# Performance work log

Hardware: AMD Instinct MI355X
Metric: run time of the kernel (lower is better)

Reference implementation:

```python
import jax, jax.numpy as jnp
import numpy as np

N, E, G = 100000, 600000, 64  # nodes, edges, graphs
F_IN, W, EPS = 32, 128, 1e-5


def setup_inputs() -> dict:
    key = jax.random.key(0)
    ks = jax.random.split(key, 16)
    p = lambda k, shape: jax.random.normal(k, shape, dtype=jnp.float32) * 0.1
    z = lambda n: jnp.zeros((n,), jnp.float32)
    o = lambda n: jnp.ones((n,), jnp.float32)
    return {
        "x": jax.random.normal(ks[0], (N, F_IN), dtype=jnp.float32),
        "edge_index": jax.random.randint(ks[1], (2, E), 0, N, dtype=jnp.int32),
        "batch": jnp.sort(jax.random.randint(ks[2], (N,), 0, G, dtype=jnp.int32)),
        # GCNConv layers
        "W1": p(ks[3], (F_IN, W)), "b1": z(W),
        "W2": p(ks[4], (W, W)), "b2": z(W),
        # mlp_first: Linear -> BN -> ReLU -> Linear
        "W3": p(ks[5], (W, W)), "b3": z(W), "g1": o(W), "be1": z(W),
        "W4": p(ks[6], (W, W)), "b4": z(W),
        # mlp: Linear -> BN -> ReLU -> Linear
        "W5": p(ks[7], (W, W // 2)), "b5": z(W // 2), "g2": o(W // 2), "be2": z(W // 2),
        "W6": p(ks[8], (W // 2, 1)), "b6": z(1),
    }


def gcn_conv(x, src, dst, Wt, b):
    # PyG GCNConv with add_self_loops=True: D^-1/2 (A+I) D^-1/2 (x W) + b
    h = x @ Wt  # [N, width]
    deg = jax.ops.segment_sum(jnp.ones(src.shape[0], x.dtype), dst, num_segments=N) + 1.0
    dinv = jax.lax.rsqrt(deg)
    norm = dinv[src] * dinv[dst]  # per-edge normalization
    agg = jax.ops.segment_sum(h[src] * norm[:, None], dst, num_segments=N)
    # self-loop term: norm for (i,i) is 1/deg[i]
    return agg + h * (dinv * dinv)[:, None] + b


def batch_norm(x, g, b):
    # training-mode BatchNorm1d (batch stats, biased var)
    mu = x.mean(axis=0)
    var = jnp.mean((x - mu) ** 2, axis=0)
    return (x - mu) * jax.lax.rsqrt(var + EPS) * g + b


def reference(x, edge_index, batch, W1, b1, W2, b2, W3, b3, g1, be1, W4, b4, W5, b5, g2, be2, W6, b6):
    src, dst = edge_index[0], edge_index[1]
    x = jax.nn.relu(gcn_conv(x, src, dst, W1, b1))
    x = jax.nn.relu(gcn_conv(x, src, dst, W2, b2))
    # mlp_first + ReLU
    x = jax.nn.relu(batch_norm(x @ W3 + b3, g1, be1)) @ W4 + b4
    x = jax.nn.relu(x)
    # global max pool over nodes per graph
    x = jax.ops.segment_max(x, batch, num_segments=G)  # [G, width]
    # final mlp
    x = jax.nn.relu(batch_norm(x @ W5 + b5, g2, be2)) @ W6 + b6
    return x[:, 0]
```

## Files before the change

### kernel.cpp

```cpp
#include <hip/hip_runtime.h>

#define N_NODES 100000
#define N_EDGES 600000
#define N_GRAPHS 64
#define EPS 1e-5f
#define SCAN_BLOCKS 391

typedef unsigned short u16;
typedef unsigned int u32;
typedef __attribute__((ext_vector_type(8))) short bf16x8;
typedef __attribute__((ext_vector_type(4))) float f32x4;

__device__ __forceinline__ float bf2f(u16 u) { return __uint_as_float(((u32)u) << 16); }
__device__ __forceinline__ u16 f2bf(float f) {
    u32 u = __float_as_uint(f);
    u += 0x7FFFu + ((u >> 16) & 1u);
    return (u16)(u >> 16);
}
__device__ __forceinline__ float2 bfx2(u32 v) {
    float2 r;
    r.x = __uint_as_float(v << 16);
    r.y = __uint_as_float(v & 0xFFFF0000u);
    return r;
}

#define WS_COUNTS   ((size_t)0)
#define WS_CURSOR   ((size_t)400384)
#define WS_POOLED   ((size_t)800768)
#define WS_BNSUM    ((size_t)833536)
#define WS_BNSUMSQ  ((size_t)834048)
#define WS_FLAG     ((size_t)834560)
#define ZERO_BYTES  ((size_t)835072)
#define WS_OFFSETS  ((size_t)835072)
#define WS_DINV     ((size_t)1235456)
#define WS_DINV2    ((size_t)1635840)
#define WS_SRCS     ((size_t)2036224)
#define WS_ZF       ((size_t)4436736)
#define WS_CANONW   ((size_t)4453120)
#define WS_BUFA     ((size_t)4578560)
#define WS_BUFB     ((size_t)30178560)

#define CW_W1 0
#define CW_B1 4096
#define CW_W2 4224
#define CW_B2 20608
#define CW_W3 20736
#define CW_B3 37120
#define CW_G1 37248
#define CW_BE1 37376
#define CW_W4 37504
#define CW_B4 53888
#define CW_W5 54016
#define CW_B5 62208
#define CW_G2 62272
#define CW_BE2 62336
#define CW_W6 62400
#define CW_B6 62464

__global__ void detect_kernel(const u32* __restrict__ xraw, int* __restrict__ flag) {
    __shared__ int cnt;
    if (threadIdx.x == 0) cnt = 0;
    __syncthreads();
    int c = 0;
    for (int i = threadIdx.x; i < 2048; i += 256) {
        u32 w = xraw[i];
        float a = fabsf(__uint_as_float((w & 0xFFFFu) << 16));
        if (a == 0.f || (a > 1e-8f && a < 1e4f)) c++;
    }
    atomicAdd(&cnt, c);
    __syncthreads();
    if (threadIdx.x == 0) *flag = (cnt > 1024) ? 1 : 0;
}

__global__ void convx_kernel(const void* __restrict__ xsrc, u16* __restrict__ dst,
                             const int* __restrict__ flag, const float* __restrict__ dinv) {
    int i = blockIdx.x * 256 + threadIdx.x;
    if (i < N_NODES * 32) {
        int r = i >> 5, c = i & 31;
        float v = (*flag) ? bf2f(((const u16*)xsrc)[i]) : ((const float*)xsrc)[i];
        dst[(size_t)(c >> 3) * (N_NODES * 8) + (size_t)r * 8 + (c & 7)] = f2bf(v * dinv[r]);
    }
}

struct SmallArgs {
    const void* src[16];
    int n[16];
    int off[16];
    int cols[16];
};
__global__ void convs_kernel(SmallArgs a, u16* __restrict__ dst, const int* __restrict__ flag) {
    int i = blockIdx.x * 256 + threadIdx.x;
    int isbf = *flag;
#pragma unroll
    for (int j = 0; j < 16; j++)
        if (i < a.n[j]) {
            u16 v = isbf ? ((const u16*)a.src[j])[i] : f2bf(((const float*)a.src[j])[i]);
            if (a.cols[j] > 0) {
                int k = i / a.cols[j];
                int n = i - k * a.cols[j];
                int Kd = a.n[j] / a.cols[j];
                dst[a.off[j] + n * Kd + k] = v;
            } else {
                dst[a.off[j] + i] = v;
            }
        }
}

__global__ void deg_kernel(const int* __restrict__ dst, int* __restrict__ counts) {
    int e = blockIdx.x * 256 + threadIdx.x;
    if (e < N_EDGES) atomicAdd(&counts[dst[e]], 1);
}

__global__ __launch_bounds__(256) void reduce_kernel(const int* __restrict__ counts,
                                                     int* __restrict__ partials) {
    int i = blockIdx.x * 256 + threadIdx.x;
    int v = (i < N_NODES) ? counts[i] : 0;
    for (int off = 32; off > 0; off >>= 1) v += __shfl_down(v, off, 64);
    __shared__ int wsum[4];
    if ((threadIdx.x & 63) == 0) wsum[threadIdx.x >> 6] = v;
    __syncthreads();
    if (threadIdx.x == 0) partials[blockIdx.x] = wsum[0] + wsum[1] + wsum[2] + wsum[3];
}

__global__ __launch_bounds__(512) void scanpart_kernel(int* __restrict__ partials) {
    __shared__ int sc[512];
    int t = threadIdx.x;
    int v = (t < SCAN_BLOCKS) ? partials[t] : 0;
    sc[t] = v;
    __syncthreads();
    for (int off = 1; off < 512; off <<= 1) {
        int u = (t >= off) ? sc[t - off] : 0;
        __syncthreads();
        sc[t] += u;
        __syncthreads();
    }
    if (t < SCAN_BLOCKS) partials[t] = sc[t] - v;
}

__global__ __launch_bounds__(256) void offsets_kernel(const int* __restrict__ counts,
                                                      const int* __restrict__ partials,
                                                      int* __restrict__ offs,
                                                      float* __restrict__ dinv) {
    int i = blockIdx.x * 256 + threadIdx.x;
    int lane = threadIdx.x & 63, wv = threadIdx.x >> 6;
    int v = (i < N_NODES) ? counts[i] : 0;
    int sv = v;
    for (int off = 1; off < 64; off <<= 1) {
        int u = __shfl_up(sv, off, 64);
        if (lane >= off) sv += u;
    }
    __shared__ int wsum[4];
    if (lane == 63) wsum[wv] = sv;
    __syncthreads();
    int wpre = 0;
    for (int w = 0; w < wv; w++) wpre += wsum[w];
    int excl = sv - v + wpre + partials[blockIdx.x];
    if (i < N_NODES) {
        offs[i] = excl;
        dinv[i] = rsqrtf((float)(v + 1));
    }
    if (i == N_NODES - 1) offs[N_NODES] = excl + v;
}

__global__ void scatter_kernel(const int* __restrict__ src, const int* __restrict__ dst,
                               const int* __restrict__ offs, int* __restrict__ cursor,
                               int* __restrict__ srcs) {
    int e = blockIdx.x * 256 + threadIdx.x;
    if (e < N_EDGES) {
        int d = dst[e];
        int p = offs[d] + atomicAdd(&cursor[d], 1);
        srcs[p] = src[e];
    }
}

__global__ __launch_bounds__(256, 8) void agg1_kernel(const u16* __restrict__ xs4,
                                                      const int* __restrict__ offs,
                                                      const int* __restrict__ srcs,
                                                      const float* __restrict__ dinv,
                                                      u16* __restrict__ axs) {
    const int p = blockIdx.x & 3;
    const int r = (blockIdx.x >> 2) * 256 + threadIdx.x;
    if (r >= N_NODES) return;
    const u16* base = xs4 + (size_t)p * (N_NODES * 8);
    float acc[8];
    {
        uint4 own = *(const uint4*)(base + (size_t)r * 8);
        u32 w4[4] = {own.x, own.y, own.z, own.w};
#pragma unroll
        for (int t = 0; t < 4; t++) {
            float2 f = bfx2(w4[t]);
            acc[2 * t] = f.x;
            acc[2 * t + 1] = f.y;
        }
    }
    const int e0 = offs[r], e1 = offs[r + 1];
    for (int e = e0; e < e1; e++) {
        int s = srcs[e];
        uint4 raw = *(const uint4*)(base + (size_t)s * 8);
        u32 w4[4] = {raw.x, raw.y, raw.z, raw.w};
#pragma unroll
        for (int t = 0; t < 4; t++) {
            float2 f = bfx2(w4[t]);
            acc[2 * t] += f.x;
            acc[2 * t + 1] += f.y;
        }
    }
    const float di = dinv[r];
    uint4 outv;
    u32* pk = (u32*)&outv;
#pragma unroll
    for (int t = 0; t < 4; t++)
        pk[t] = (u32)f2bf(acc[2 * t] * di) | ((u32)f2bf(acc[2 * t + 1] * di) << 16);
    *(uint4*)(axs + (size_t)r * 32 + p * 8) = outv;
}

__global__ __launch_bounds__(256, 8) void agg2_kernel(const u16* __restrict__ P2,
                                                      const int* __restrict__ offs,
                                                      const int* __restrict__ srcs,
                                                      const float* __restrict__ dinv,
                                                      const u16* __restrict__ b2,
                                                      u16* __restrict__ x2) {
    const int p = blockIdx.x & 7;
    const int t = threadIdx.x;
    const int r = (blockIdx.x >> 3) * 128 + (t >> 1);
    const int half = t & 1;
    if (r >= N_NODES) return;
    const u16* base = P2 + (size_t)p * (N_NODES * 16) + half * 8;
    float acc[8];
    {
        uint4 own = *(const uint4*)(base + (size_t)r * 16);
        u32 w4[4] = {own.x, own.y, own.z, own.w};
#pragma unroll
        for (int j = 0; j < 4; j++) {
            float2 f = bfx2(w4[j]);
            acc[2 * j] = f.x;
            acc[2 * j + 1] = f.y;
        }
    }
    const int e0 = offs[r], e1 = offs[r + 1];
    for (int e = e0; e < e1; e++) {
        int s = srcs[e];
        uint4 raw = *(const uint4*)(base + (size_t)s * 16);
        u32 w4[4] = {raw.x, raw.y, raw.z, raw.w};
#pragma unroll
        for (int j = 0; j < 4; j++) {
            float2 f = bfx2(w4[j]);
            acc[2 * j] += f.x;
            acc[2 * j + 1] += f.y;
        }
    }
    const float di = dinv[r];
    uint4 bb = *(const uint4*)(b2 + p * 16 + half * 8);
    u32 bw[4] = {bb.x, bb.y, bb.z, bb.w};
    uint4 outv;
    u32* pk = (u32*)&outv;
#pragma unroll
    for (int j = 0; j < 4; j++) {
        float2 fb = bfx2(bw[j]);
        float vx = fmaxf(fmaf(acc[2 * j], di, fb.x), 0.f);
        float vy = fmaxf(fmaf(acc[2 * j + 1], di, fb.y), 0.f);
        pk[j] = (u32)f2bf(vx) | ((u32)f2bf(vy) << 16);
    }
    *(uint4*)(x2 + (size_t)r * 128 + p * 16 + half * 8) = outv;
}

__global__ __launch_bounds__(256, 3) void gemmx_kernel(
    const u16* __restrict__ axs, const u16* __restrict__ W1t, const u16* __restrict__ b1,
    const u16* __restrict__ W2t, u16* __restrict__ P2, const float* __restrict__ dinv, int M) {
    __shared__ __align__(16) u16 ldsA[128 * 40];
    __shared__ __align__(16) u16 ldsB[128 * 136];

    const int tid = threadIdx.x;
    const int wave = tid >> 6;
    const int lane = tid & 63;
    const int l15 = lane & 15;
    const int quad = lane >> 4;
    const int row0 = blockIdx.x * 128 + wave * 32;

    {
        const u32* g = (const u32*)W1t;
        u32* l = (u32*)ldsA;
        for (int i = tid; i < 128 * 16; i += 256) {
            int n = i >> 4, j = i & 15;
            l[n * 20 + j] = g[i];
        }
    }
    {
        const u32* g = (const u32*)W2t;
        u32* l = (u32*)ldsB;
        for (int i = tid; i < 128 * 64; i += 256) {
            int n = i >> 6, j = i & 63;
            l[n * 68 + j] = g[i];
        }
    }

    uint4 gr1[2];
#pragma unroll
    for (int rt = 0; rt < 2; rt++) {
        int r = min(row0 + rt * 16 + l15, M - 1);
        gr1[rt] = *(const uint4*)(axs + (size_t)r * 32 + quad * 8);
    }
    __syncthreads();

    f32x4 acc1[2][8];
#pragma unroll
    for (int rt = 0; rt < 2; rt++)
#pragma unroll
        for (int nt = 0; nt < 8; nt++) acc1[rt][nt] = {0.f, 0.f, 0.f, 0.f};
#pragma unroll
    for (int nt = 0; nt < 8; nt++) {
        bf16x8 bf = *(const bf16x8*)&ldsA[(nt * 16 + l15) * 40 + quad * 8];
        acc1[0][nt] = __builtin_amdgcn_mfma_f32_16x16x32_bf16(
            __builtin_bit_cast(bf16x8, gr1[0]), bf, acc1[0][nt], 0, 0, 0);
        acc1[1][nt] = __builtin_amdgcn_mfma_f32_16x16x32_bf16(
            __builtin_bit_cast(bf16x8, gr1[1]), bf, acc1[1][nt], 0, 0, 0);
    }
    __syncthreads();

    float bcol[8];
#pragma unroll
    for (int nt = 0; nt < 8; nt++) bcol[nt] = bf2f(b1[nt * 16 + l15]);
    u16* tb = ldsA + wave * 1280;
    uint4 gr2[2][4];
#pragma unroll
    for (int kt = 0; kt < 4; kt++) {
#pragma unroll
        for (int rt = 0; rt < 2; rt++)
#pragma unroll
            for (int c2 = 0; c2 < 2; c2++) {
                int nt = 2 * kt + c2;
#pragma unroll
                for (int i = 0; i < 4; i++) {
                    float v = fmaxf(acc1[rt][nt][i] + bcol[nt], 0.f);
                    tb[(rt * 16 + quad * 4 + i) * 40 + c2 * 16 + l15] = f2bf(v);
                }
            }
#pragma unroll
        for (int rt = 0; rt < 2; rt++)
            gr2[rt][kt] = *(const uint4*)&tb[(rt * 16 + l15) * 40 + quad * 8];
    }

    f32x4 acc2[2][8];
#pragma unroll
    for (int rt = 0; rt < 2; rt++)
#pragma unroll
        for (int nt = 0; nt < 8; nt++) acc2[rt][nt] = {0.f, 0.f, 0.f, 0.f};
#pragma unroll
    for (int kt = 0; kt < 4; kt++) {
#pragma unroll
        for (int nt = 0; nt < 8; nt++) {
            bf16x8 bf = *(const bf16x8*)&ldsB[(nt * 16 + l15) * 136 + kt * 32 + quad * 8];
            acc2[0][nt] = __builtin_amdgcn_mfma_f32_16x16x32_bf16(
                __builtin_bit_cast(bf16x8, gr2[0][kt]), bf, acc2[0][nt], 0, 0, 0);
            acc2[1][nt] = __builtin_amdgcn_mfma_f32_16x16x32_bf16(
                __builtin_bit_cast(bf16x8, gr2[1][kt]), bf, acc2[1][nt], 0, 0, 0);
        }
    }

#pragma unroll
    for (int rt = 0; rt < 2; rt++)
#pragma unroll
        for (int i = 0; i < 4; i++) {
            int r = row0 + rt * 16 + quad * 4 + i;
            if (r < M) {
                float ds = dinv[r];
#pragma unroll
                for (int nt = 0; nt < 8; nt++)
                    P2[(size_t)nt * (N_NODES * 16) + (size_t)r * 16 + l15] =
                        f2bf(acc2[rt][nt][i] * ds);
            }
        }
}

template <int K, int IN_MODE, int OUT_MODE>
__global__ __launch_bounds__(256, 3) void mgemm_kernel(
    const u16* __restrict__ A, const u16* __restrict__ Wt, const u16* __restrict__ bias,
    u16* __restrict__ C, const float* __restrict__ scl, const float* __restrict__ shf,
    float* __restrict__ bn_sum, float* __restrict__ bn_sumsq, const int* __restrict__ batch,
    u32* __restrict__ pooled, int M) {
    constexpr int KP = K + 8;
    __shared__ __align__(16) u16 Wl[128 * KP];
    __shared__ float csum[128], csumsq[128];

    const int tid = threadIdx.x;
    const int wave = tid >> 6;
    const int lane = tid & 63;
    const int l15 = lane & 15;
    const int quad = lane >> 4;
    const int row0 = blockIdx.x * 128 + wave * 32;

    {
        const u32* g = (const u32*)Wt;
        u32* l = (u32*)Wl;
        for (int i = tid; i < 128 * (K / 2); i += 256) {
            int n = i / (K / 2), j = i - n * (K / 2);
            l[n * (KP / 2) + j] = g[i];
        }
    }
    if (OUT_MODE == 1 && tid < 128) { csum[tid] = 0.f; csumsq[tid] = 0.f; }
    __syncthreads();

    f32x4 acc[2][8];
#pragma unroll
    for (int rt = 0; rt < 2; rt++)
#pragma unroll
        for (int nt = 0; nt < 8; nt++) acc[rt][nt] = {0.f, 0.f, 0.f, 0.f};

#pragma unroll
    for (int k0 = 0; k0 < K; k0 += 32) {
        bf16x8 af[2];
        if (IN_MODE == 0) {
#pragma unroll
            for (int rt = 0; rt < 2; rt++) {
                int r = min(row0 + rt * 16 + l15, M - 1);
                af[rt] = *(const bf16x8*)(A + (size_t)r * K + k0 + quad * 8);
            }
        } else {
            float s8[8], h8[8];
#pragma unroll
            for (int t = 0; t < 8; t++) {
                s8[t] = scl[k0 + quad * 8 + t];
                h8[t] = shf[k0 + quad * 8 + t];
            }
#pragma unroll
            for (int rt = 0; rt < 2; rt++) {
                int r = min(row0 + rt * 16 + l15, M - 1);
                uint4 raw = *(const uint4*)(A + (size_t)r * K + k0 + quad * 8);
                u32 w4[4] = {raw.x, raw.y, raw.z, raw.w};
                bf16x8 tmp;
#pragma unroll
                for (int t = 0; t < 4; t++) {
                    float2 f = bfx2(w4[t]);
                    f.x = fmaxf(fmaf(f.x, s8[2 * t], h8[2 * t]), 0.f);
                    f.y = fmaxf(fmaf(f.y, s8[2 * t + 1], h8[2 * t + 1]), 0.f);
                    tmp[2 * t] = (short)f2bf(f.x);
                    tmp[2 * t + 1] = (short)f2bf(f.y);
                }
                af[rt] = tmp;
            }
        }
#pragma unroll
        for (int nt = 0; nt < 8; nt++) {
            bf16x8 bf = *(const bf16x8*)&Wl[(nt * 16 + l15) * KP + k0 + quad * 8];
            acc[0][nt] = __builtin_amdgcn_mfma_f32_16x16x32_bf16(af[0], bf, acc[0][nt], 0, 0, 0);
            acc[1][nt] = __builtin_amdgcn_mfma_f32_16x16x32_bf16(af[1], bf, acc[1][nt], 0, 0, 0);
        }
    }

    if (OUT_MODE == 1) {
        float b[8], s[8], sq[8];
#pragma unroll
        for (int nt = 0; nt < 8; nt++) {
            b[nt] = bf2f(bias[nt * 16 + l15]);
            s[nt] = 0.f;
            sq[nt] = 0.f;
        }
#pragma unroll
        for (int rt = 0; rt < 2; rt++)
#pragma unroll
            for (int i = 0; i < 4; i++) {
                int r = row0 + rt * 16 + quad * 4 + i;
                if (r < M) {
                    u16* cp = C + (size_t)r * 128 + l15;
#pragma unroll
                    for (int nt = 0; nt < 8; nt++) {
                        float v = acc[rt][nt][i] + b[nt];
                        s[nt] += v;
                        sq[nt] += v * v;
                        cp[nt * 16] = f2bf(v);
                    }
                }
            }
#pragma unroll
        for (int nt = 0; nt < 8; nt++) {
            atomicAdd(&csum[nt * 16 + l15], s[nt]);
            atomicAdd(&csumsq[nt * 16 + l15], sq[nt]);
        }
        __syncthreads();
        if (tid < 128) {
            atomicAdd(&bn_sum[tid], csum[tid]);
            atomicAdd(&bn_sumsq[tid], csumsq[tid]);
        }
    } else {
        float b[8];
#pragma unroll
        for (int nt = 0; nt < 8; nt++) b[nt] = bf2f(bias[nt * 16 + l15]);
        float cur[8];
#pragma unroll
        for (int nt = 0; nt < 8; nt++) cur[nt] = 0.f;
        int curg = -1;
#pragma unroll
        for (int rt = 0; rt < 2; rt++)
#pragma unroll
            for (int i = 0; i < 4; i++) {
                int r = row0 + rt * 16 + quad * 4 + i;
                if (r < M) {
                    int g = batch[r];
                    if (g != curg) {
                        if (curg >= 0) {
                            u32* bp = pooled + curg * 128 + l15;
#pragma unroll
                            for (int nt = 0; nt < 8; nt++)
                                if (cur[nt] > 0.f)
                                    atomicMax(&bp[nt * 16], __float_as_uint(cur[nt]));
                        }
                        curg = g;
#pragma unroll
                        for (int nt = 0; nt < 8; nt++) cur[nt] = 0.f;
                    }
#pragma unroll
                    for (int nt = 0; nt < 8; nt++)
                        cur[nt] = fmaxf(cur[nt], fmaxf(acc[rt][nt][i] + b[nt], 0.f));
                }
            }
        if (curg >= 0) {
            u32* bp = pooled + curg * 128 + l15;
#pragma unroll
            for (int nt = 0; nt < 8; nt++)
                if (cur[nt] > 0.f) atomicMax(&bp[nt * 16], __float_as_uint(cur[nt]));
        }
    }
}

__global__ void bnstats_kernel(float* __restrict__ bn_sum, float* __restrict__ bn_sumsq,
                               const u16* __restrict__ g1, const u16* __restrict__ be1) {
    int c = threadIdx.x;
    if (c < 128) {
        float mu = bn_sum[c] / (float)N_NODES;
        float var = bn_sumsq[c] / (float)N_NODES - mu * mu;
        float rstd = rsqrtf(var + EPS);
        float sc = rstd * bf2f(g1[c]);
        bn_sum[c] = sc;
        bn_sumsq[c] = bf2f(be1[c]) - mu * sc;
    }
}

__global__ __launch_bounds__(256) void head1_kernel(const u32* __restrict__ pooled,
                                                    const u16* __restrict__ W5,
                                                    const u16* __restrict__ b5,
                                                    float* __restrict__ zf) {
    __shared__ float red[4][64];
    int g = blockIdx.x;
    int c = threadIdx.x & 63;
    int kq = threadIdx.x >> 6;
    const u32* prow = pooled + g * 128;
    float p = 0.f;
    for (int k = kq * 32; k < kq * 32 + 32; k++)
        p = fmaf(__uint_as_float(prow[k]), bf2f(W5[k * 64 + c]), p);
    red[kq][c] = p;
    __syncthreads();
    if (kq == 0) zf[g * 64 + c] = red[0][c] + red[1][c] + red[2][c] + red[3][c] + bf2f(b5[c]);
}

__global__ __launch_bounds__(64) void head2_kernel(const float* __restrict__ zf,
                                                   const u16* __restrict__ g2,
                                                   const u16* __restrict__ be2,
                                                   const u16* __restrict__ W6,
                                                   const u16* __restrict__ b6,
                                                   void* __restrict__ outv,
                                                   const int* __restrict__ flag) {
    __shared__ float Z[64][65];
    __shared__ float sc[64], sh[64], w6[64];
    int t = threadIdx.x;
    for (int idx = t; idx < 4096; idx += 64) Z[idx >> 6][idx & 63] = zf[idx];
    w6[t] = bf2f(W6[t]);
    __syncthreads();
    {
        float s = 0.f, sq = 0.f;
        for (int g = 0; g < 64; g++) {
            float v = Z[g][t];
            s += v;
            sq += v * v;
        }
        float mu = s * (1.f / 64.f);
        float var = sq * (1.f / 64.f) - mu * mu;
        float rstd = rsqrtf(var + EPS);
        float scale = rstd * bf2f(g2[t]);
        sc[t] = scale;
        sh[t] = bf2f(be2[t]) - mu * scale;
    }
    __syncthreads();
    float o = 0.f;
    for (int c = 0; c < 64; c++)
        o = fmaf(fmaxf(fmaf(Z[t][c], sc[c], sh[c]), 0.f), w6[c], o);
    float res = o + bf2f(b6[0]);
    if (*flag)
        ((u16*)outv)[t] = f2bf(res);
    else
        ((float*)outv)[t] = res;
}

extern "C" void kernel_launch(void* const* d_in, const int* in_sizes, int n_in, void* d_out,
                              int out_size, void* d_ws, size_t ws_size, hipStream_t stream) {
    const void* x = d_in[0];
    const int* ei = (const int*)d_in[1];
    const int* bat = (const int*)d_in[2];

    char* ws = (char*)d_ws;
    int* counts = (int*)(ws + WS_COUNTS);
    int* cursor = (int*)(ws + WS_CURSOR);
    u32* pooled = (u32*)(ws + WS_POOLED);
    float* bnsum = (float*)(ws + WS_BNSUM);
    float* bnssq = (float*)(ws + WS_BNSUMSQ);
    int* flag = (int*)(ws + WS_FLAG);
    int* offs = (int*)(ws + WS_OFFSETS);
    float* dinv = (float*)(ws + WS_DINV);
    int* partials = (int*)(ws + WS_DINV2);
    int* srcs = (int*)(ws + WS_SRCS);
    float* zf = (float*)(ws + WS_ZF);
    u16* cw = (u16*)(ws + WS_CANONW);
    u16* P2 = (u16*)(ws + WS_BUFA);
    u16* xs4 = (u16*)(ws + WS_BUFB);
    u16* axs = (u16*)(ws + WS_BUFB) + 3200000;
    u16* x2 = (u16*)(ws + WS_BUFB);

    const int* esrc = ei;
    const int* edst = ei + N_EDGES;

    hipMemsetAsync(ws, 0, ZERO_BYTES, stream);
    detect_kernel<<<1, 256, 0, stream>>>((const u32*)x, flag);

    SmallArgs sa;
    const int cw_off[16] = {CW_W1, CW_B1, CW_W2, CW_B2, CW_W3, CW_B3, CW_G1, CW_BE1,
                            CW_W4, CW_B4, CW_W5, CW_B5, CW_G2, CW_BE2, CW_W6, CW_B6};
    const int cw_n[16] = {4096, 128, 16384, 128, 16384, 128, 128, 128,
                          16384, 128, 8192, 64, 64, 64, 64, 1};
    const int cw_c[16] = {128, 0, 128, 0, 128, 0, 0, 0, 128, 0, 0, 0, 0, 0, 0, 0};
    for (int j = 0; j < 16; j++) {
        sa.src[j] = d_in[3 + j];
        sa.n[j] = cw_n[j];
        sa.off[j] = cw_off[j];
        sa.cols[j] = cw_c[j];
    }
    convs_kernel<<<64, 256, 0, stream>>>(sa, cw, flag);

    deg_kernel<<<(N_EDGES + 255) / 256, 256, 0, stream>>>(edst, counts);
    reduce_kernel<<<SCAN_BLOCKS, 256, 0, stream>>>(counts, partials);
    scanpart_kernel<<<1, 512, 0, stream>>>(partials);
    offsets_kernel<<<SCAN_BLOCKS, 256, 0, stream>>>(counts, partials, offs, dinv);
    scatter_kernel<<<(N_EDGES + 255) / 256, 256, 0, stream>>>(esrc, edst, offs, cursor, srcs);
    convx_kernel<<<(N_NODES * 32 + 255) / 256, 256, 0, stream>>>(x, xs4, flag, dinv);

    const int gb = (N_NODES + 127) / 128;
    agg1_kernel<<<4 * SCAN_BLOCKS, 256, 0, stream>>>(xs4, offs, srcs, dinv, axs);
    gemmx_kernel<<<gb, 256, 0, stream>>>(axs, cw + CW_W1, cw + CW_B1, cw + CW_W2, P2, dinv,
                                         N_NODES);
    agg2_kernel<<<8 * gb, 256, 0, stream>>>(P2, offs, srcs, dinv, cw + CW_B2, x2);
    mgemm_kernel<128, 0, 1><<<gb, 256, 0, stream>>>(x2, cw + CW_W3, cw + CW_B3, x2, nullptr,
                                                    nullptr, bnsum, bnssq, nullptr, nullptr,
                                                    N_NODES);
    bnstats_kernel<<<1, 128, 0, stream>>>(bnsum, bnssq, cw + CW_G1, cw + CW_BE1);
    mgemm_kernel<128, 1, 2><<<gb, 256, 0, stream>>>(x2, cw + CW_W4, cw + CW_B4, nullptr, bnsum,
                                                    bnssq, nullptr, nullptr, bat, pooled,
                                                    N_NODES);
    head1_kernel<<<N_GRAPHS, 256, 0, stream>>>(pooled, cw + CW_W5, cw + CW_B5, zf);
    head2_kernel<<<1, 64, 0, stream>>>(zf, cw + CW_G2, cw + CW_BE2, cw + CW_W6, cw + CW_B6,
                                       d_out, flag);
}
```

Baseline: 367.9 us.

## Split MLP GEMM into specialized kernels with prefetched A, vector stores, LDS pooling

The templated GEMM is replaced by two specialized kernels. Both issue all A-row loads before staging the weights into LDS, so global latency overlaps the weight copy. The BN-statistics kernel swaps MFMA operands so each lane holds 4 consecutive columns of one row, which allows packed 8-byte stores and shuffle-reduced column sums instead of per-element LDS atomics. The pooling kernel accumulates per-graph maxima in shared memory when a block spans few graphs, which cuts global atomicMax traffic at the cost of extra LDS and a sync.

```diff
diff --git a/kernel.cpp b/kernel.cpp
--- a/kernel.cpp
+++ b/kernel.cpp
@@ -372,13 +372,10 @@
         }
 }
 
-template <int K, int IN_MODE, int OUT_MODE>
-__global__ __launch_bounds__(256, 3) void mgemm_kernel(
+__global__ __launch_bounds__(256, 3) void gemm3_kernel(
     const u16* __restrict__ A, const u16* __restrict__ Wt, const u16* __restrict__ bias,
-    u16* __restrict__ C, const float* __restrict__ scl, const float* __restrict__ shf,
-    float* __restrict__ bn_sum, float* __restrict__ bn_sumsq, const int* __restrict__ batch,
-    u32* __restrict__ pooled, int M) {
-    constexpr int KP = K + 8;
+    u16* __restrict__ C, float* __restrict__ bn_sum, float* __restrict__ bn_sumsq, int M) {
+    constexpr int KP = 136;
     __shared__ __align__(16) u16 Wl[128 * KP];
     __shared__ float csum[128], csumsq[128];
 
@@ -389,15 +386,29 @@
     const int quad = lane >> 4;
     const int row0 = blockIdx.x * 128 + wave * 32;
 
+    uint4 ra[2][4];
+    int nd[2];
+#pragma unroll
+    for (int rt = 0; rt < 2; rt++) {
+        nd[rt] = row0 + rt * 16 + l15;
+        int r = min(nd[rt], M - 1);
+        const u16* ap = A + (size_t)r * 128 + quad * 8;
+#pragma unroll
+        for (int kt = 0; kt < 4; kt++) ra[rt][kt] = *(const uint4*)(ap + kt * 32);
+    }
+
     {
         const u32* g = (const u32*)Wt;
         u32* l = (u32*)Wl;
-        for (int i = tid; i < 128 * (K / 2); i += 256) {
-            int n = i / (K / 2), j = i - n * (K / 2);
-            l[n * (KP / 2) + j] = g[i];
-        }
-    }
-    if (OUT_MODE == 1 && tid < 128) { csum[tid] = 0.f; csumsq[tid] = 0.f; }
+        for (int i = tid; i < 128 * 64; i += 256) {
+            int n = i >> 6, j = i & 63;
+            l[n * 68 + j] = g[i];
+        }
+    }
+    if (tid < 128) {
+        csum[tid] = 0.f;
+        csumsq[tid] = 0.f;
+    }
     __syncthreads();
 
     f32x4 acc[2][8];
@@ -407,117 +418,192 @@
         for (int nt = 0; nt < 8; nt++) acc[rt][nt] = {0.f, 0.f, 0.f, 0.f};
 
 #pragma unroll
-    for (int k0 = 0; k0 < K; k0 += 32) {
+    for (int kt = 0; kt < 4; kt++) {
+        bf16x8 a0 = __builtin_bit_cast(bf16x8, ra[0][kt]);
+        bf16x8 a1 = __builtin_bit_cast(bf16x8, ra[1][kt]);
+#pragma unroll
+        for (int nt = 0; nt < 8; nt++) {
+            bf16x8 wf = *(const bf16x8*)&Wl[(nt * 16 + l15) * KP + kt * 32 + quad * 8];
+            acc[0][nt] = __builtin_amdgcn_mfma_f32_16x16x32_bf16(wf, a0, acc[0][nt], 0, 0, 0);
+            acc[1][nt] = __builtin_amdgcn_mfma_f32_16x16x32_bf16(wf, a1, acc[1][nt], 0, 0, 0);
+        }
+    }
+
+    const bool ok0 = nd[0] < M, ok1 = nd[1] < M;
+#pragma unroll
+    for (int nt = 0; nt < 8; nt++) {
+        uint2 braw = *(const uint2*)(bias + nt * 16 + quad * 4);
+        float2 f0 = bfx2(braw.x), f1 = bfx2(braw.y);
+        float bb[4] = {f0.x, f0.y, f1.x, f1.y};
+        float v0[4], v1[4];
+#pragma unroll
+        for (int i = 0; i < 4; i++) {
+            v0[i] = ok0 ? (acc[0][nt][i] + bb[i]) : 0.f;
+            v1[i] = ok1 ? (acc[1][nt][i] + bb[i]) : 0.f;
+        }
+        if (ok0) {
+            uint2 st;
+            st.x = (u32)f2bf(v0[0]) | ((u32)f2bf(v0[1]) << 16);
+            st.y = (u32)f2bf(v0[2]) | ((u32)f2bf(v0[3]) << 16);
+            *(uint2*)(C + (size_t)nd[0] * 128 + nt * 16 + quad * 4) = st;
+        }
+        if (ok1) {
+            uint2 st;
+            st.x = (u32)f2bf(v1[0]) | ((u32)f2bf(v1[1]) << 16);
+            st.y = (u32)f2bf(v1[2]) | ((u32)f2bf(v1[3]) << 16);
+            *(uint2*)(C + (size_t)nd[1] * 128 + nt * 16 + quad * 4) = st;
+        }
+#pragma unroll
+        for (int i = 0; i < 4; i++) {
+            float s = v0[i] + v1[i];
+            float q = v0[i] * v0[i] + v1[i] * v1[i];
+#pragma unroll
+            for (int m = 1; m < 16; m <<= 1) {
+                s += __shfl_xor(s, m);
+                q += __shfl_xor(q, m);
+            }
+            if (l15 == 0) {
+                atomicAdd(&csum[nt * 16 + quad * 4 + i], s);
+                atomicAdd(&csumsq[nt * 16 + quad * 4 + i], q);
+            }
+        }
+    }
+    __syncthreads();
+    if (tid < 128) {
+        atomicAdd(&bn_sum[tid], csum[tid]);
+        atomicAdd(&bn_sumsq[tid], csumsq[tid]);
+    }
+}
+
+__global__ __launch_bounds__(256, 3) void gemm4_kernel(
+    const u16* __restrict__ A, const u16* __restrict__ Wt, const u16* __restrict__ bias,
+    const float* __restrict__ scl, const float* __restrict__ shf,
+    const int* __restrict__ batch, u32* __restrict__ pooled, int M) {
+    constexpr int KP = 136;
+    __shared__ __align__(16) u16 Wl[128 * KP];
+    __shared__ u32 lmax[4 * 128];
+
+    const int tid = threadIdx.x;
+    const int wave = tid >> 6;
+    const int lane = tid & 63;
+    const int l15 = lane & 15;
+    const int quad = lane >> 4;
+    const int row0 = blockIdx.x * 128 + wave * 32;
+
+    uint4 ra[2][4];
+#pragma unroll
+    for (int rt = 0; rt < 2; rt++) {
+        int r = min(row0 + rt * 16 + l15, M - 1);
+        const u16* ap = A + (size_t)r * 128 + quad * 8;
+#pragma unroll
+        for (int kt = 0; kt < 4; kt++) ra[rt][kt] = *(const uint4*)(ap + kt * 32);
+    }
+
+    {
+        const u32* g = (const u32*)Wt;
+        u32* l = (u32*)Wl;
+        for (int i = tid; i < 128 * 64; i += 256) {
+            int n = i >> 6, j = i & 63;
+            l[n * 68 + j] = g[i];
+        }
+    }
+    for (int i = tid; i < 512; i += 256) lmax[i] = 0u;
+
+    const int base = blockIdx.x * 128;
+    const int gfirst = batch[min(base, M - 1)];
+    const int glast = batch[min(base + 127, M - 1)];
+    const bool fast = (glast - gfirst) < 4;
+    __syncthreads();
+
+    f32x4 acc[2][8];
+#pragma unroll
+    for (int rt = 0; rt < 2; rt++)
+#pragma unroll
+        for (int nt = 0; nt < 8; nt++) acc[rt][nt] = {0.f, 0.f, 0.f, 0.f};
+
+#pragma unroll
+    for (int kt = 0; kt < 4; kt++) {
+        float s8[8], h8[8];
+#pragma unroll
+        for (int t = 0; t < 8; t++) {
+            s8[t] = scl[kt * 32 + quad * 8 + t];
+            h8[t] = shf[kt * 32 + quad * 8 + t];
+        }
         bf16x8 af[2];
-        if (IN_MODE == 0) {
-#pragma unroll
-            for (int rt = 0; rt < 2; rt++) {
-                int r = min(row0 + rt * 16 + l15, M - 1);
-                af[rt] = *(const bf16x8*)(A + (size_t)r * K + k0 + quad * 8);
+#pragma unroll
+        for (int rt = 0; rt < 2; rt++) {
+            u32 w4[4] = {ra[rt][kt].x, ra[rt][kt].y, ra[rt][kt].z, ra[rt][kt].w};
+            bf16x8 tmp;
+#pragma unroll
+            for (int t = 0; t < 4; t++) {
+                float2 f = bfx2(w4[t]);
+                f.x = fmaxf(fmaf(f.x, s8[2 * t], h8[2 * t]), 0.f);
+                f.y = fmaxf(fmaf(f.y, s8[2 * t + 1], h8[2 * t + 1]), 0.f);
+                tmp[2 * t] = (short)f2bf(f.x);
+                tmp[2 * t + 1] = (short)f2bf(f.y);
             }
-        } else {
-            float s8[8], h8[8];
-#pragma unroll
-            for (int t = 0; t < 8; t++) {
-                s8[t] = scl[k0 + quad * 8 + t];
-                h8[t] = shf[k0 + quad * 8 + t];
-            }
-#pragma unroll
-            for (int rt = 0; rt < 2; rt++) {
-                int r = min(row0 + rt * 16 + l15, M - 1);
-                uint4 raw = *(const uint4*)(A + (size_t)r * K + k0 + quad * 8);
-                u32 w4[4] = {raw.x, raw.y, raw.z, raw.w};
-                bf16x8 tmp;
-#pragma unroll
-                for (int t = 0; t < 4; t++) {
-                    float2 f = bfx2(w4[t]);
-                    f.x = fmaxf(fmaf(f.x, s8[2 * t], h8[2 * t]), 0.f);
-                    f.y = fmaxf(fmaf(f.y, s8[2 * t + 1], h8[2 * t + 1]), 0.f);
-                    tmp[2 * t] = (short)f2bf(f.x);
-                    tmp[2 * t + 1] = (short)f2bf(f.y);
-                }
-                af[rt] = tmp;
-            }
+            af[rt] = tmp;
         }
 #pragma unroll
         for (int nt = 0; nt < 8; nt++) {
-            bf16x8 bf = *(const bf16x8*)&Wl[(nt * 16 + l15) * KP + k0 + quad * 8];
+            bf16x8 bf = *(const bf16x8*)&Wl[(nt * 16 + l15) * KP + kt * 32 + quad * 8];
             acc[0][nt] = __builtin_amdgcn_mfma_f32_16x16x32_bf16(af[0], bf, acc[0][nt], 0, 0, 0);
             acc[1][nt] = __builtin_amdgcn_mfma_f32_16x16x32_bf16(af[1], bf, acc[1][nt], 0, 0, 0);
         }
     }
 
-    if (OUT_MODE == 1) {
-        float b[8], s[8], sq[8];
-#pragma unroll
-        for (int nt = 0; nt < 8; nt++) {
-            b[nt] = bf2f(bias[nt * 16 + l15]);
-            s[nt] = 0.f;
-            sq[nt] = 0.f;
-        }
-#pragma unroll
-        for (int rt = 0; rt < 2; rt++)
-#pragma unroll
-            for (int i = 0; i < 4; i++) {
-                int r = row0 + rt * 16 + quad * 4 + i;
-                if (r < M) {
-                    u16* cp = C + (size_t)r * 128 + l15;
-#pragma unroll
-                    for (int nt = 0; nt < 8; nt++) {
-                        float v = acc[rt][nt][i] + b[nt];
-                        s[nt] += v;
-                        sq[nt] += v * v;
-                        cp[nt * 16] = f2bf(v);
+    float b[8];
+#pragma unroll
+    for (int nt = 0; nt < 8; nt++) b[nt] = bf2f(bias[nt * 16 + l15]);
+    float cur[8];
+#pragma unroll
+    for (int nt = 0; nt < 8; nt++) cur[nt] = 0.f;
+    int curg = -1;
+#pragma unroll
+    for (int rt = 0; rt < 2; rt++)
+#pragma unroll
+        for (int i = 0; i < 4; i++) {
+            int r = row0 + rt * 16 + quad * 4 + i;
+            if (r < M) {
+                int g = batch[r];
+                if (g != curg) {
+                    if (curg >= 0) {
+#pragma unroll
+                        for (int nt = 0; nt < 8; nt++)
+                            if (cur[nt] > 0.f) {
+                                u32 bits = __float_as_uint(cur[nt]);
+                                if (fast)
+                                    atomicMax(&lmax[(curg - gfirst) * 128 + nt * 16 + l15], bits);
+                                else
+                                    atomicMax(&pooled[curg * 128 + nt * 16 + l15], bits);
+                            }
                     }
+                    curg = g;
+#pragma unroll
+                    for (int nt = 0; nt < 8; nt++) cur[nt] = 0.f;
                 }
+#pragma unroll
+                for (int nt = 0; nt < 8; nt++)
+                    cur[nt] = fmaxf(cur[nt], fmaxf(acc[rt][nt][i] + b[nt], 0.f));
             }
-#pragma unroll
-        for (int nt = 0; nt < 8; nt++) {
-            atomicAdd(&csum[nt * 16 + l15], s[nt]);
-            atomicAdd(&csumsq[nt * 16 + l15], sq[nt]);
-        }
-        __syncthreads();
-        if (tid < 128) {
-            atomicAdd(&bn_sum[tid], csum[tid]);
-            atomicAdd(&bn_sumsq[tid], csumsq[tid]);
-        }
-    } else {
-        float b[8];
-#pragma unroll
-        for (int nt = 0; nt < 8; nt++) b[nt] = bf2f(bias[nt * 16 + l15]);
-        float cur[8];
-#pragma unroll
-        for (int nt = 0; nt < 8; nt++) cur[nt] = 0.f;
-        int curg = -1;
-#pragma unroll
-        for (int rt = 0; rt < 2; rt++)
-#pragma unroll
-            for (int i = 0; i < 4; i++) {
-                int r = row0 + rt * 16 + quad * 4 + i;
-                if (r < M) {
-                    int g = batch[r];
-                    if (g != curg) {
-                        if (curg >= 0) {
-                            u32* bp = pooled + curg * 128 + l15;
-#pragma unroll
-                            for (int nt = 0; nt < 8; nt++)
-                                if (cur[nt] > 0.f)
-                                    atomicMax(&bp[nt * 16], __float_as_uint(cur[nt]));
-                        }
-                        curg = g;
-#pragma unroll
-                        for (int nt = 0; nt < 8; nt++) cur[nt] = 0.f;
-                    }
-#pragma unroll
-                    for (int nt = 0; nt < 8; nt++)
-                        cur[nt] = fmaxf(cur[nt], fmaxf(acc[rt][nt][i] + b[nt], 0.f));
-                }
+        }
+    if (curg >= 0) {
+#pragma unroll
+        for (int nt = 0; nt < 8; nt++)
+            if (cur[nt] > 0.f) {
+                u32 bits = __float_as_uint(cur[nt]);
+                if (fast)
+                    atomicMax(&lmax[(curg - gfirst) * 128 + nt * 16 + l15], bits);
+                else
+                    atomicMax(&pooled[curg * 128 + nt * 16 + l15], bits);
             }
-        if (curg >= 0) {
-            u32* bp = pooled + curg * 128 + l15;
-#pragma unroll
-            for (int nt = 0; nt < 8; nt++)
-                if (cur[nt] > 0.f) atomicMax(&bp[nt * 16], __float_as_uint(cur[nt]));
+    }
+    __syncthreads();
+    if (fast) {
+        int ngr = glast - gfirst + 1;
+        for (int i = tid; i < ngr * 128; i += 256) {
+            u32 v = lmax[i];
+            if (v) atomicMax(&pooled[gfirst * 128 + i], v);
         }
     }
 }
@@ -646,13 +732,10 @@
     gemmx_kernel<<<gb, 256, 0, stream>>>(axs, cw + CW_W1, cw + CW_B1, cw + CW_W2, P2, dinv,
                                          N_NODES);
     agg2_kernel<<<8 * gb, 256, 0, stream>>>(P2, offs, srcs, dinv, cw + CW_B2, x2);
-    mgemm_kernel<128, 0, 1><<<gb, 256, 0, stream>>>(x2, cw + CW_W3, cw + CW_B3, x2, nullptr,
-                                                    nullptr, bnsum, bnssq, nullptr, nullptr,
-                                                    N_NODES);
+    gemm3_kernel<<<gb, 256, 0, stream>>>(x2, cw + CW_W3, cw + CW_B3, x2, bnsum, bnssq, N_NODES);
     bnstats_kernel<<<1, 128, 0, stream>>>(bnsum, bnssq, cw + CW_G1, cw + CW_BE1);
-    mgemm_kernel<128, 1, 2><<<gb, 256, 0, stream>>>(x2, cw + CW_W4, cw + CW_B4, nullptr, bnsum,
-                                                    bnssq, nullptr, nullptr, bat, pooled,
-                                                    N_NODES);
+    gemm4_kernel<<<gb, 256, 0, stream>>>(x2, cw + CW_W4, cw + CW_B4, bnsum, bnssq, bat, pooled,
+                                         N_NODES);
     head1_kernel<<<N_GRAPHS, 256, 0, stream>>>(pooled, cw + CW_W5, cw + CW_B5, zf);
     head2_kernel<<<1, 64, 0, stream>>>(zf, cw + CW_G2, cw + CW_BE2, cw + CW_W6, cw + CW_B6,
                                        d_out, flag);
```

Result: faster. 333.6 us (-9.3%).
